# Performance work log

Hardware: AMD Instinct MI355X
Metric: run time of the kernel (lower is better)

## Reference

```python
import jax, jax.numpy as jnp
import numpy as np

B, L, H, S, IN = 64, 64, 128, 64, 16  # batch, embedding_seq_len, hidden, seq_num, input_size


def setup_inputs() -> dict:
    key = jax.random.key(0)
    k = jax.random.split(key, 8)
    trip = jax.random.normal(k[0], (B, 256, IN), dtype=jnp.float32)
    valid_len = jax.random.randint(k[1], (B,), 0, 256)
    embedding = jax.random.normal(k[2], (B, L, H), dtype=jnp.float32)
    # gates: Linear(2H -> 4H), xavier-uniform weight
    lim_g = float(np.sqrt(6.0 / (2 * H + 4 * H)))
    W_gates = jax.random.uniform(k[3], (2 * H, 4 * H), minval=-lim_g, maxval=lim_g, dtype=jnp.float32)
    b_gates = jax.random.uniform(k[4], (4 * H,), minval=-1.0 / np.sqrt(2 * H), maxval=1.0 / np.sqrt(2 * H), dtype=jnp.float32)
    # linear: Linear(H -> input_size)
    lim_l = float(np.sqrt(6.0 / (H + IN)))
    W_lin = jax.random.uniform(k[5], (H, IN), minval=-lim_l, maxval=lim_l, dtype=jnp.float32)
    b_lin = jax.random.uniform(k[6], (IN,), minval=-1.0 / np.sqrt(H), maxval=1.0 / np.sqrt(H), dtype=jnp.float32)
    return {"trip": trip, "valid_len": valid_len, "embedding": embedding,
            "W_gates": W_gates, "b_gates": b_gates, "W_lin": W_lin, "b_lin": b_lin}


def _gate_update(inp, c, W_gates, b_gates):
    g = inp @ W_gates + b_gates
    f, i, o, cand = jnp.split(g, 4, axis=-1)
    c_new = jax.nn.sigmoid(f) * c + jax.nn.sigmoid(i) * jnp.tanh(cand)  # broadcasts [B,1,H] vs [B,L,H] at step 0
    h_new = jax.nn.sigmoid(o) * jnp.tanh(c_new)
    return c_new, h_new


def reference(trip, valid_len, embedding, W_gates, b_gates, W_lin, b_lin):
    x = trip  # sampler pass-through
    b, l, h = embedding.shape
    c0 = jnp.zeros((b, l, h), dtype=embedding.dtype)
    h0 = jnp.zeros((b, l, h), dtype=embedding.dtype)
    # step 0: gates on [embedding[:, :1], h[:, :1]] -> [B,1,4H], broadcast update
    inp0 = jnp.concatenate([embedding[:, :1, :], h0[:, :1, :]], axis=-1)
    c1, h1 = _gate_update(inp0, c0, W_gates, b_gates)

    def step(carry, _):
        c, hh = carry
        inp = jnp.concatenate([c, hh], axis=-1)  # [B,L,2H]
        c_new, h_new = _gate_update(inp, c, W_gates, b_gates)
        return (c_new, h_new), c_new

    (_, _), cs = jax.lax.scan(step, (c1, h1), None, length=S - 1)  # cs: [S-1,B,L,H]
    c_all = jnp.concatenate([c1[None], cs], axis=0)          # [S,B,L,H]
    c_all = jnp.transpose(c_all, (1, 0, 2, 3)).reshape(b, S * l, h)  # cat along dim=-2
    out = c_all @ W_lin + b_lin  # [B, S*L, IN]
    return (x, out)
```

## Files before the change

kernel.cpp:

```cpp
#include <hip/hip_runtime.h>

typedef _Float16 half2_t __attribute__((ext_vector_type(2)));

#define NBATCH 64
#define LLEN   64
#define HDIM   128
#define NSTEP  64
#define NIN    16
#define HISTP  132

__device__ __forceinline__ float sigf(float x) { return 1.f / (1.f + __expf(-x)); }

__device__ __forceinline__ unsigned int h2u(half2_t h) {
    union { half2_t h; unsigned int u; } x; x.h = h; return x.u;
}
__device__ __forceinline__ half2_t u2h(unsigned int u) {
    union { half2_t h; unsigned int u; } x; x.u = u; return x.h;
}

__global__ __launch_bounds__(256) void copy_trip_k(const float4* __restrict__ src,
                                                   float4* __restrict__ dst) {
    int i = blockIdx.x * 256 + threadIdx.x;
    dst[i] = src[i];
}

__global__ __launch_bounds__(512) void recur_k(
    const float* __restrict__ emb, const float* __restrict__ Wg,
    const float* __restrict__ bg,  const float* __restrict__ Wl,
    const float* __restrict__ bl,  float* __restrict__ out) {
    __shared__ __align__(16) unsigned int pack_s[2][128];
    __shared__ float g_s[512];
    __shared__ float hist[NSTEP * HISTP];
    __shared__ float Wl_s[HDIM * NIN];
    __shared__ float proj_s[NSTEP * NIN];

    const int b = blockIdx.x, t = threadIdx.x;

    unsigned int Whu[128];
    #pragma unroll
    for (int k = 0; k < 128; ++k) {
        float w0 = Wg[(2 * k + 0) * 512 + t];
        float w1 = Wg[(2 * k + 1) * 512 + t];
        half2_t hp = { (_Float16)w0, (_Float16)w1 };
        Whu[k] = h2u(hp);
    }
    #pragma unroll
    for (int k = 0; k < 128; ++k) asm volatile("" : "+v"(Whu[k]));

    for (int i = t; i < HDIM * NIN; i += 512) Wl_s[i] = Wl[i];

    if (t < 64) {
        float e0 = emb[b * (LLEN * HDIM) + 2 * t + 0];
        float e1 = emb[b * (LLEN * HDIM) + 2 * t + 1];
        half2_t hp = { (_Float16)e0, (_Float16)e1 };
        pack_s[0][t] = h2u(hp);
    } else if (t < 128) {
        pack_s[0][t] = 0u;
    }
    float c_reg = 0.f;
    const float bgj = bg[t];
    __syncthreads();

    for (int s = 0; s < NSTEP; ++s) {
        const uint4* p4 = (const uint4*)pack_s[s & 1];
        float a0 = bgj, a1 = 0.f;
        #pragma unroll
        for (int q = 0; q < 32; ++q) {
            uint4 u = p4[q];
            a0 = __builtin_amdgcn_fdot2(u2h(u.x), u2h(Whu[4 * q + 0]), a0, false);
            a1 = __builtin_amdgcn_fdot2(u2h(u.y), u2h(Whu[4 * q + 1]), a1, false);
            a0 = __builtin_amdgcn_fdot2(u2h(u.z), u2h(Whu[4 * q + 2]), a0, false);
            a1 = __builtin_amdgcn_fdot2(u2h(u.w), u2h(Whu[4 * q + 3]), a1, false);
        }
        g_s[t] = a0 + a1;
        __syncthreads();

        if (t < HDIM) {
            float fg = sigf(g_s[t]);
            float ig = sigf(g_s[HDIM + t]);
            float og = sigf(g_s[2 * HDIM + t]);
            float cd = tanhf(g_s[3 * HDIM + t]);
            float c_new = fg * c_reg + ig * cd;
            float h_new = og * tanhf(c_new);
            c_reg = c_new;
            hist[s * HISTP + t] = c_new;
            float c_o = __shfl_xor(c_new, 1);
            float h_o = __shfl_xor(h_new, 1);
            if ((t & 1) == 0) {
                half2_t cp = { (_Float16)c_new, (_Float16)c_o };
                half2_t hp = { (_Float16)h_new, (_Float16)h_o };
                int nb = (s + 1) & 1;
                pack_s[nb][(t >> 1)]      = h2u(cp);
                pack_s[nb][64 + (t >> 1)] = h2u(hp);
            }
        }
        __syncthreads();
    }

    #pragma unroll
    for (int r = 0; r < 2; ++r) {
        int p = t * 2 + r;
        int s = p >> 4, i = p & 15;
        float acc = bl[i];
        const float4* c4 = (const float4*)&hist[s * HISTP];
        #pragma unroll 8
        for (int h4 = 0; h4 < HDIM / 4; ++h4) {
            float4 cv = c4[h4];
            int h = h4 * 4;
            acc = fmaf(cv.x, Wl_s[(h + 0) * NIN + i], acc);
            acc = fmaf(cv.y, Wl_s[(h + 1) * NIN + i], acc);
            acc = fmaf(cv.z, Wl_s[(h + 2) * NIN + i], acc);
            acc = fmaf(cv.w, Wl_s[(h + 3) * NIN + i], acc);
        }
        proj_s[s * NIN + i] = acc;
    }
    __syncthreads();

    float4* ob = (float4*)(out + (size_t)b * (NSTEP * LLEN * NIN));
    const float4* pj = (const float4*)proj_s;
    for (int u = t; u < NSTEP * LLEN * NIN / 4; u += 512) {
        int row = u >> 2;
        int s = row >> 6;
        int ib = u & 3;
        ob[u] = pj[s * 4 + ib];
    }
}

extern "C" void kernel_launch(void* const* d_in, const int* in_sizes, int n_in,
                              void* d_out, int out_size, void* d_ws, size_t ws_size,
                              hipStream_t stream) {
    const float* trip = (const float*)d_in[0];
    const float* emb  = (const float*)d_in[2];
    const float* Wg   = (const float*)d_in[3];
    const float* bgp  = (const float*)d_in[4];
    const float* Wlp  = (const float*)d_in[5];
    const float* blp  = (const float*)d_in[6];
    float* out = (float*)d_out;

    copy_trip_k<<<256, 256, 0, stream>>>((const float4*)trip, (float4*)out);
    recur_k<<<NBATCH, 512, 0, stream>>>(emb, Wg, bgp, Wlp, blp, out + 262144);
}
```

Baseline: 90.66 us.

## Split gate dot-product K across two thread halves and move output broadcast to separate kernel

The recurrence block grows from 512 to 1024 threads, and each half computes a partial dot product over half of the 256-element input. The partials are summed with the bias in the gate-activation phase. This halves the serial FMA chain per step and the weight registers per thread. The broadcast write of the projected output is moved from the 64-block recurrence kernel into a wide separate expand kernel, so the large store spreads over many CUs, at the cost of an extra launch and a workspace round trip.

```diff
diff --git a/kernel.cpp b/kernel.cpp
--- a/kernel.cpp
+++ b/kernel.cpp
@@ -3,7 +3,6 @@
 typedef _Float16 half2_t __attribute__((ext_vector_type(2)));
 
 #define NBATCH 64
-#define LLEN   64
 #define HDIM   128
 #define NSTEP  64
 #define NIN    16
@@ -24,62 +23,60 @@
     dst[i] = src[i];
 }
 
-__global__ __launch_bounds__(512) void recur_k(
+__global__ __launch_bounds__(1024) void recur_k(
     const float* __restrict__ emb, const float* __restrict__ Wg,
     const float* __restrict__ bg,  const float* __restrict__ Wl,
-    const float* __restrict__ bl,  float* __restrict__ out) {
+    const float* __restrict__ bl,  float* __restrict__ proj_ws) {
     __shared__ __align__(16) unsigned int pack_s[2][128];
-    __shared__ float g_s[512];
+    __shared__ float gpart[2][512];
     __shared__ float hist[NSTEP * HISTP];
     __shared__ float Wl_s[HDIM * NIN];
-    __shared__ float proj_s[NSTEP * NIN];
+    __shared__ float bg_s[512];
 
     const int b = blockIdx.x, t = threadIdx.x;
+    const int j = t & 511, kh = t >> 9;
 
-    unsigned int Whu[128];
+    unsigned int Wr[64];
     #pragma unroll
-    for (int k = 0; k < 128; ++k) {
-        float w0 = Wg[(2 * k + 0) * 512 + t];
-        float w1 = Wg[(2 * k + 1) * 512 + t];
+    for (int k = 0; k < 64; ++k) {
+        float w0 = Wg[(kh * 128 + 2 * k + 0) * 512 + j];
+        float w1 = Wg[(kh * 128 + 2 * k + 1) * 512 + j];
         half2_t hp = { (_Float16)w0, (_Float16)w1 };
-        Whu[k] = h2u(hp);
+        Wr[k] = h2u(hp);
     }
-    #pragma unroll
-    for (int k = 0; k < 128; ++k) asm volatile("" : "+v"(Whu[k]));
 
-    for (int i = t; i < HDIM * NIN; i += 512) Wl_s[i] = Wl[i];
-
+    if (t < 512) bg_s[t] = bg[t];
+    for (int i = t; i < HDIM * NIN; i += 1024) Wl_s[i] = Wl[i];
     if (t < 64) {
-        float e0 = emb[b * (LLEN * HDIM) + 2 * t + 0];
-        float e1 = emb[b * (LLEN * HDIM) + 2 * t + 1];
+        float e0 = emb[b * (64 * HDIM) + 2 * t + 0];
+        float e1 = emb[b * (64 * HDIM) + 2 * t + 1];
         half2_t hp = { (_Float16)e0, (_Float16)e1 };
         pack_s[0][t] = h2u(hp);
     } else if (t < 128) {
         pack_s[0][t] = 0u;
     }
     float c_reg = 0.f;
-    const float bgj = bg[t];
     __syncthreads();
 
     for (int s = 0; s < NSTEP; ++s) {
-        const uint4* p4 = (const uint4*)pack_s[s & 1];
-        float a0 = bgj, a1 = 0.f;
+        const uint4* p4 = (const uint4*)&pack_s[s & 1][kh * 64];
+        float a0 = 0.f, a1 = 0.f;
         #pragma unroll
-        for (int q = 0; q < 32; ++q) {
+        for (int q = 0; q < 16; ++q) {
             uint4 u = p4[q];
-            a0 = __builtin_amdgcn_fdot2(u2h(u.x), u2h(Whu[4 * q + 0]), a0, false);
-            a1 = __builtin_amdgcn_fdot2(u2h(u.y), u2h(Whu[4 * q + 1]), a1, false);
-            a0 = __builtin_amdgcn_fdot2(u2h(u.z), u2h(Whu[4 * q + 2]), a0, false);
-            a1 = __builtin_amdgcn_fdot2(u2h(u.w), u2h(Whu[4 * q + 3]), a1, false);
+            a0 = __builtin_amdgcn_fdot2(u2h(u.x), u2h(Wr[4 * q + 0]), a0, false);
+            a1 = __builtin_amdgcn_fdot2(u2h(u.y), u2h(Wr[4 * q + 1]), a1, false);
+            a0 = __builtin_amdgcn_fdot2(u2h(u.z), u2h(Wr[4 * q + 2]), a0, false);
+            a1 = __builtin_amdgcn_fdot2(u2h(u.w), u2h(Wr[4 * q + 3]), a1, false);
         }
-        g_s[t] = a0 + a1;
+        gpart[kh][j] = a0 + a1;
         __syncthreads();
 
         if (t < HDIM) {
-            float fg = sigf(g_s[t]);
-            float ig = sigf(g_s[HDIM + t]);
-            float og = sigf(g_s[2 * HDIM + t]);
-            float cd = tanhf(g_s[3 * HDIM + t]);
+            float fg = sigf(gpart[0][t]       + gpart[1][t]       + bg_s[t]);
+            float ig = sigf(gpart[0][128 + t] + gpart[1][128 + t] + bg_s[128 + t]);
+            float og = sigf(gpart[0][256 + t] + gpart[1][256 + t] + bg_s[256 + t]);
+            float cd = tanhf(gpart[0][384 + t] + gpart[1][384 + t] + bg_s[384 + t]);
             float c_new = fg * c_reg + ig * cd;
             float h_new = og * tanhf(c_new);
             c_reg = c_new;
@@ -97,10 +94,8 @@
         __syncthreads();
     }
 
-    #pragma unroll
-    for (int r = 0; r < 2; ++r) {
-        int p = t * 2 + r;
-        int s = p >> 4, i = p & 15;
+    {
+        int s = t >> 4, i = t & 15;
         float acc = bl[i];
         const float4* c4 = (const float4*)&hist[s * HISTP];
         #pragma unroll 8
@@ -112,18 +107,18 @@
             acc = fmaf(cv.z, Wl_s[(h + 2) * NIN + i], acc);
             acc = fmaf(cv.w, Wl_s[(h + 3) * NIN + i], acc);
         }
-        proj_s[s * NIN + i] = acc;
+        proj_ws[b * 1024 + t] = acc;
     }
-    __syncthreads();
+}
 
-    float4* ob = (float4*)(out + (size_t)b * (NSTEP * LLEN * NIN));
-    const float4* pj = (const float4*)proj_s;
-    for (int u = t; u < NSTEP * LLEN * NIN / 4; u += 512) {
-        int row = u >> 2;
-        int s = row >> 6;
-        int ib = u & 3;
-        ob[u] = pj[s * 4 + ib];
-    }
+__global__ __launch_bounds__(256) void expand_k(const float* __restrict__ proj_ws,
+                                                float* __restrict__ out) {
+    int blk = blockIdx.x;
+    int t = threadIdx.x;
+    const float4* pj = (const float4*)(proj_ws + blk * 16);
+    float4 v = pj[t & 3];
+    float4* ob = (float4*)(out + (size_t)blk * 1024);
+    ob[t] = v;
 }
 
 extern "C" void kernel_launch(void* const* d_in, const int* in_sizes, int n_in,
@@ -136,7 +131,9 @@
     const float* Wlp  = (const float*)d_in[5];
     const float* blp  = (const float*)d_in[6];
     float* out = (float*)d_out;
+    float* proj_ws = (float*)d_ws;
 
     copy_trip_k<<<256, 256, 0, stream>>>((const float4*)trip, (float4*)out);
-    recur_k<<<NBATCH, 512, 0, stream>>>(emb, Wg, bgp, Wlp, blp, out + 262144);
+    recur_k<<<NBATCH, 1024, 0, stream>>>(emb, Wg, bgp, Wlp, blp, proj_ws);
+    expand_k<<<NBATCH * NSTEP, 256, 0, stream>>>(proj_ws, out + 262144);
 }
```

Result: slower. 92.83 us (+2.4%).
